# Optimization experiments

Hardware: AMD Instinct MI355X
Metric: run time of the kernel (lower is better)

The kernel has to match this reference:

```python
import jax, jax.numpy as jnp
import numpy as np

DIM = 768
NUM_HEADS = 12
HEAD_DIM = DIM // NUM_HEADS
SCALE = HEAD_DIM ** -0.5


def setup_inputs() -> dict:
    key = jax.random.key(0)
    k1, k2, k3, k4 = jax.random.split(key, 4)
    B, N, C = 4, 2048, DIM
    x = jax.random.normal(k1, (B, N, C), dtype=jnp.float32)
    # nn.Linear(dim, 3*dim, bias=False): weight shape (3C, C), y = x @ W^T
    w_qkv = jax.random.normal(k2, (3 * C, C), dtype=jnp.float32) * (C ** -0.5)
    # nn.Linear(dim, dim) with default bias=True
    w_proj = jax.random.normal(k3, (C, C), dtype=jnp.float32) * (C ** -0.5)
    b_proj = jax.random.normal(k4, (C,), dtype=jnp.float32) * 0.02
    return {"x": x, "w_qkv": w_qkv, "w_proj": w_proj, "b_proj": b_proj}


def reference(x, w_qkv, w_proj, b_proj):
    B, N, C = x.shape
    H, D = NUM_HEADS, HEAD_DIM
    qkv = jnp.einsum('bnc,oc->bno', x, w_qkv)  # (B, N, 3C)
    qkv = qkv.reshape(B, N, 3, H, D).transpose(2, 0, 3, 1, 4)  # (3, B, H, N, D)
    q, k, v = qkv[0], qkv[1], qkv[2]
    attn = jnp.einsum('bhnd,bhmd->bhnm', q, k) * jnp.float32(SCALE)  # (B,H,N,N)
    attn = jax.nn.softmax(attn, axis=-1)
    out = jnp.einsum('bhnm,bhmd->bhnd', attn, v)  # (B,H,N,D)
    out = out.transpose(0, 2, 1, 3).reshape(B, N, C)
    out = jnp.einsum('bnc,oc->bno', out, w_proj) + b_proj
    return out
```

## Files before the change

### kernel.cpp

```cpp
#include <hip/hip_runtime.h>
#include <math.h>

#define B_ 4
#define N_ 2048
#define C_ 768
#define H_ 12
#define D_ 64
#define SCALE_ 0.125f

typedef unsigned short u16;
typedef unsigned int u32;
typedef short s16x8 __attribute__((ext_vector_type(8)));
typedef float f32x4 __attribute__((ext_vector_type(4)));

__device__ __forceinline__ u16 f2bf(float f) {
    union { float f; unsigned int u; } v; v.f = f;
    unsigned int r = (v.u + 0x7fffu + ((v.u >> 16) & 1u)) >> 16;
    return (u16)r;
}

__global__ __launch_bounds__(256) void cvt_bf16(const float4* __restrict__ src,
                                                ushort4* __restrict__ dst, int n4)
{
    int i = blockIdx.x * blockDim.x + threadIdx.x;
    const int stride = gridDim.x * blockDim.x;
    for (; i < n4; i += stride) {
        float4 v = src[i];
        ushort4 o;
        o.x = f2bf(v.x); o.y = f2bf(v.y); o.z = f2bf(v.z); o.w = f2bf(v.w);
        dst[i] = o;
    }
}

template<bool OUT_BF16, bool BIAS, bool QSCALE>
__global__ __launch_bounds__(256) void gemm_mfma(const u16* __restrict__ A,
                                                 const u16* __restrict__ Bm,
                                                 const float* __restrict__ bias,
                                                 void* __restrict__ Cout,
                                                 int M, int N, int K)
{
    __shared__ u16 As[128][40];
    __shared__ u16 Bs[128][40];
    const int tid  = threadIdx.x;
    const int wv   = tid >> 6;
    const int lane = tid & 63;
    const int lr   = lane & 15;
    const int lq   = lane >> 4;
    const int wm   = (wv >> 1) * 64, wn = (wv & 1) * 64;
    const int row0 = blockIdx.y * 128, col0 = blockIdx.x * 128;

    f32x4 acc[4][4];
    #pragma unroll
    for (int i = 0; i < 4; i++)
        #pragma unroll
        for (int j = 0; j < 4; j++) { f32x4 z = {0.f,0.f,0.f,0.f}; acc[i][j] = z; }

    const int srow = tid >> 1, scol = (tid & 1) * 16;
    const u16* Ag = A + (size_t)(row0 + srow) * K + scol;
    const u16* Bg = Bm + (size_t)(col0 + srow) * K + scol;

    for (int k0 = 0; k0 < K; k0 += 32) {
        *(s16x8*)&As[srow][scol]     = *(const s16x8*)(Ag + k0);
        *(s16x8*)&As[srow][scol + 8] = *(const s16x8*)(Ag + k0 + 8);
        *(s16x8*)&Bs[srow][scol]     = *(const s16x8*)(Bg + k0);
        *(s16x8*)&Bs[srow][scol + 8] = *(const s16x8*)(Bg + k0 + 8);
        __syncthreads();
        s16x8 af[4], bfr[4];
        #pragma unroll
        for (int i = 0; i < 4; i++) af[i]  = *(const s16x8*)&As[wm + 16*i + lr][lq*8];
        #pragma unroll
        for (int j = 0; j < 4; j++) bfr[j] = *(const s16x8*)&Bs[wn + 16*j + lr][lq*8];
        #pragma unroll
        for (int i = 0; i < 4; i++)
            #pragma unroll
            for (int j = 0; j < 4; j++)
                acc[i][j] = __builtin_amdgcn_mfma_f32_16x16x32_bf16(af[i], bfr[j], acc[i][j], 0, 0, 0);
        __syncthreads();
    }

    #pragma unroll
    for (int i = 0; i < 4; i++) {
        #pragma unroll
        for (int j = 0; j < 4; j++) {
            const int col = col0 + wn + 16*j + lr;
            float bv = BIAS ? bias[col] : 0.f;
            #pragma unroll
            for (int r = 0; r < 4; r++) {
                const int row = row0 + wm + 16*i + lq*4 + r;
                float v = acc[i][j][r] + bv;
                if (QSCALE && col < C_) v *= SCALE_;
                if (OUT_BF16) ((u16*)Cout)[(size_t)row * N + col] = f2bf(v);
                else          ((float*)Cout)[(size_t)row * N + col] = v;
            }
        }
    }
}

__global__ __launch_bounds__(256, 4) void attn_mfma(const u16* __restrict__ qkv,
                                                    u16* __restrict__ attout)
{
    __shared__ u16 Ks[64][72];
    __shared__ u16 Vt[64][72];
    __shared__ u16 Ps[128][72];

    const int tid  = threadIdx.x;
    const int wv   = tid >> 6;
    const int lane = tid & 63;
    const int lr   = lane & 15;
    const int lq   = lane >> 4;
    const int n0   = blockIdx.x * 128;
    const int bh   = blockIdx.y, b = bh / H_, h = bh % H_;
    const size_t rs = 3 * C_;

    const u16* Qg = qkv + ((size_t)b * N_ + n0) * rs + h * D_;
    const u16* Kg = qkv + ((size_t)b * N_) * rs + C_ + h * D_;
    const u16* Vg = Kg + C_;

    s16x8 qf[2][2];
    #pragma unroll
    for (int i = 0; i < 2; i++)
        #pragma unroll
        for (int kk = 0; kk < 2; kk++)
            qf[i][kk] = *(const s16x8*)(Qg + (size_t)(32*wv + 16*i + lr) * rs + kk*32 + lq*8);

    f32x4 oacc[2][4];
    float li[2][4];
    #pragma unroll
    for (int i = 0; i < 2; i++) {
        #pragma unroll
        for (int j = 0; j < 4; j++) { f32x4 z = {0.f,0.f,0.f,0.f}; oacc[i][j] = z; }
        #pragma unroll
        for (int r = 0; r < 4; r++) li[i][r] = 0.f;
    }

    const int skey = tid >> 2, sd0 = (tid & 3) * 16;
    const int vc = tid & 7, vp = tid >> 3;
    const int vkey0 = 2 * vp, vd0 = vc * 8;
    const int vcol0 = (vkey0 + 8 * vc) & 63;

    for (int t = 0; t < N_ / 64; t++) {
        __syncthreads();
        const u16* ksrc = Kg + (size_t)(t * 64 + skey) * rs + sd0;
        *(s16x8*)&Ks[skey][sd0]     = *(const s16x8*)(ksrc);
        *(s16x8*)&Ks[skey][sd0 + 8] = *(const s16x8*)(ksrc + 8);
        const u16* vsrc = Vg + (size_t)(t * 64 + vkey0) * rs + vd0;
        s16x8 v0 = *(const s16x8*)(vsrc);
        s16x8 v1 = *(const s16x8*)(vsrc + rs);
        #pragma unroll
        for (int u = 0; u < 8; u++) {
            u32 pk = (u32)(u16)v0[u] | ((u32)(u16)v1[u] << 16);
            *(u32*)&Vt[vd0 + u][vcol0] = pk;
        }
        __syncthreads();

        f32x4 sacc[2][4];
        #pragma unroll
        for (int i = 0; i < 2; i++)
            #pragma unroll
            for (int j = 0; j < 4; j++) { f32x4 z = {0.f,0.f,0.f,0.f}; sacc[i][j] = z; }
        #pragma unroll
        for (int kk = 0; kk < 2; kk++) {
            s16x8 bk[4];
            #pragma unroll
            for (int j = 0; j < 4; j++)
                bk[j] = *(const s16x8*)&Ks[16*j + lr][kk*32 + lq*8];
            #pragma unroll
            for (int j = 0; j < 4; j++) {
                sacc[0][j] = __builtin_amdgcn_mfma_f32_16x16x32_bf16(qf[0][kk], bk[j], sacc[0][j], 0, 0, 0);
                sacc[1][j] = __builtin_amdgcn_mfma_f32_16x16x32_bf16(qf[1][kk], bk[j], sacc[1][j], 0, 0, 0);
            }
        }

        #pragma unroll
        for (int i = 0; i < 2; i++)
            #pragma unroll
            for (int j = 0; j < 4; j++)
                #pragma unroll
                for (int r = 0; r < 4; r++) {
                    const float p = __expf(sacc[i][j][r]);
                    li[i][r] += p;
                    Ps[32*wv + 16*i + lq*4 + r][16*j + lr] = f2bf(p);
                }

        #pragma unroll
        for (int kk = 0; kk < 2; kk++) {
            s16x8 ap0 = *(const s16x8*)&Ps[32*wv      + lr][kk*32 + lq*8];
            s16x8 ap1 = *(const s16x8*)&Ps[32*wv + 16 + lr][kk*32 + lq*8];
            #pragma unroll
            for (int j2 = 0; j2 < 4; j2++) {
                const int pb = ((kk*4 + lq) + 2*j2 + (lr >> 3)) & 7;
                s16x8 bv = *(const s16x8*)&Vt[16*j2 + lr][pb * 8];
                oacc[0][j2] = __builtin_amdgcn_mfma_f32_16x16x32_bf16(ap0, bv, oacc[0][j2], 0, 0, 0);
                oacc[1][j2] = __builtin_amdgcn_mfma_f32_16x16x32_bf16(ap1, bv, oacc[1][j2], 0, 0, 0);
            }
        }
    }

    #pragma unroll
    for (int i = 0; i < 2; i++) {
        #pragma unroll
        for (int r = 0; r < 4; r++) {
            float s = li[i][r];
            #pragma unroll
            for (int mask = 1; mask < 16; mask <<= 1)
                s += __shfl_xor(s, mask);
            const float inv = 1.f / s;
            const int row = n0 + 32*wv + 16*i + lq*4 + r;
            #pragma unroll
            for (int j2 = 0; j2 < 4; j2++)
                attout[((size_t)(b * N_ + row)) * C_ + h * D_ + 16*j2 + lr] =
                    f2bf(oacc[i][j2][r] * inv);
        }
    }
}

extern "C" void kernel_launch(void* const* d_in, const int* in_sizes, int n_in,
                              void* d_out, int out_size, void* d_ws, size_t ws_size,
                              hipStream_t stream) {
    const float* x      = (const float*)d_in[0];
    const float* w_qkv  = (const float*)d_in[1];
    const float* w_proj = (const float*)d_in[2];
    const float* b_proj = (const float*)d_in[3];
    float* out = (float*)d_out;

    const int NX = B_ * N_ * C_;
    const int NWQ = 3 * C_ * C_;
    const int NWP = C_ * C_;
    const int NQKV = B_ * N_ * 3 * C_;

    u16* xb   = (u16*)d_ws;
    u16* wqb  = xb + NX;
    u16* wpb  = wqb + NWQ;
    u16* qkvb = wpb + NWP;
    u16* attb = qkvb + NQKV;

    dim3 blk(256);

    cvt_bf16<<<512, blk, 0, stream>>>((const float4*)x, (ushort4*)xb, NX / 4);
    cvt_bf16<<<256, blk, 0, stream>>>((const float4*)w_qkv, (ushort4*)wqb, NWQ / 4);
    cvt_bf16<<<128, blk, 0, stream>>>((const float4*)w_proj, (ushort4*)wpb, NWP / 4);

    const int M = B_ * N_;
    gemm_mfma<true, false, true><<<dim3((3*C_)/128, M/128), blk, 0, stream>>>(
        xb, wqb, nullptr, qkvb, M, 3*C_, C_);

    attn_mfma<<<dim3(N_/128, B_ * H_), blk, 0, stream>>>(qkvb, attb);

    gemm_mfma<false, true, false><<<dim3(C_/128, M/128), blk, 0, stream>>>(
        attb, wpb, b_proj, out, M, C_, C_);
}
```

Before: 252.1 us.

## Use direct global-to-LDS loads in GEMM, prefetch K/V, exp2 softmax with transposed scores

GEMM tiles are now staged with global_load_lds into an XOR-swizzled unpadded LDS layout, and the projection GEMM uses 64-row tiles so more blocks are launched. The attention kernel prefetches the next K/V tile into registers during compute and computes S transposed so each lane holds consecutive keys. That lets P be packed into bf16 pairs with perm and stored as 8-byte writes, and the row-sum reduction becomes two shuffles. The log2(e) factor is folded into the Q scale so exp2 can be used, and the occupancy hint is lowered from 4 to 3 to make room for the prefetch registers. Softmax still skips max-subtraction, so it relies on bounded scores.

```diff
diff --git a/kernel.cpp b/kernel.cpp
--- a/kernel.cpp
+++ b/kernel.cpp
@@ -6,17 +6,31 @@
 #define C_ 768
 #define H_ 12
 #define D_ 64
-#define SCALE_ 0.125f
+#define QKSCALE_ 0.18033688011112042f
 
 typedef unsigned short u16;
 typedef unsigned int u32;
 typedef short s16x8 __attribute__((ext_vector_type(8)));
 typedef float f32x4 __attribute__((ext_vector_type(4)));
+typedef u32 u32x2 __attribute__((ext_vector_type(2)));
 
 __device__ __forceinline__ u16 f2bf(float f) {
-    union { float f; unsigned int u; } v; v.f = f;
-    unsigned int r = (v.u + 0x7fffu + ((v.u >> 16) & 1u)) >> 16;
+    union { float f; u32 u; } v; v.f = f;
+    u32 r = (v.u + 0x7fffu + ((v.u >> 16) & 1u)) >> 16;
     return (u16)r;
+}
+
+__device__ __forceinline__ u32 pkbf(float a, float b) {
+    union { float f; u32 u; } ua, ub; ua.f = a; ub.f = b;
+    u32 ra = ua.u + 0x7fffu + ((ua.u >> 16) & 1u);
+    u32 rb = ub.u + 0x7fffu + ((ub.u >> 16) & 1u);
+    return __builtin_amdgcn_perm(rb, ra, 0x07060302u);
+}
+
+__device__ __forceinline__ void gl_lds16(const u16* g, u16* l) {
+    __builtin_amdgcn_global_load_lds(
+        (__attribute__((address_space(1))) void*)g,
+        (__attribute__((address_space(3))) void*)l, 16, 0, 0);
 }
 
 __global__ __launch_bounds__(256) void cvt_bf16(const float4* __restrict__ src,
@@ -32,46 +46,61 @@
     }
 }
 
-template<bool OUT_BF16, bool BIAS, bool QSCALE>
+template<int BM, bool OUT_BF16, bool BIAS, bool QSCALE>
 __global__ __launch_bounds__(256) void gemm_mfma(const u16* __restrict__ A,
                                                  const u16* __restrict__ Bm,
                                                  const float* __restrict__ bias,
                                                  void* __restrict__ Cout,
                                                  int M, int N, int K)
 {
-    __shared__ u16 As[128][40];
-    __shared__ u16 Bs[128][40];
+    constexpr int MF = BM / 32;
+    __shared__ __align__(16) u16 As[BM * 32];
+    __shared__ __align__(16) u16 Bs[128 * 32];
     const int tid  = threadIdx.x;
     const int wv   = tid >> 6;
     const int lane = tid & 63;
     const int lr   = lane & 15;
     const int lq   = lane >> 4;
-    const int wm   = (wv >> 1) * 64, wn = (wv & 1) * 64;
-    const int row0 = blockIdx.y * 128, col0 = blockIdx.x * 128;
-
-    f32x4 acc[4][4];
-    #pragma unroll
-    for (int i = 0; i < 4; i++)
+    const int wm   = (wv >> 1) * (BM / 2);
+    const int wn   = (wv & 1) * 64;
+    const int row0 = blockIdx.y * BM, col0 = blockIdx.x * 128;
+
+    f32x4 acc[MF][4];
+    #pragma unroll
+    for (int i = 0; i < MF; i++)
         #pragma unroll
         for (int j = 0; j < 4; j++) { f32x4 z = {0.f,0.f,0.f,0.f}; acc[i][j] = z; }
 
-    const int srow = tid >> 1, scol = (tid & 1) * 16;
-    const u16* Ag = A + (size_t)(row0 + srow) * K + scol;
-    const u16* Bg = Bm + (size_t)(col0 + srow) * K + scol;
+    const int srow   = lane >> 2;
+    const int schunk = (((lane & 3) ^ ((lane >> 3) & 3)) * 8);
+
+    const int arow_base = (BM == 128) ? 32 * wv : 16 * wv;
+    const u16* gA0 = A + (size_t)(row0 + arow_base + srow) * K + schunk;
+    const u16* gA1 = gA0 + (size_t)16 * K;
+    const u16* gB0 = Bm + (size_t)(col0 + 32 * wv + srow) * K + schunk;
+    const u16* gB1 = gB0 + (size_t)16 * K;
+    u16* lA0 = As + arow_base * 32;
+    u16* lA1 = lA0 + 16 * 32;
+    u16* lB0 = Bs + (32 * wv) * 32;
+    u16* lB1 = lB0 + 16 * 32;
+
+    const int ppos = (lq ^ ((lr >> 1) & 3)) * 8;
 
     for (int k0 = 0; k0 < K; k0 += 32) {
-        *(s16x8*)&As[srow][scol]     = *(const s16x8*)(Ag + k0);
-        *(s16x8*)&As[srow][scol + 8] = *(const s16x8*)(Ag + k0 + 8);
-        *(s16x8*)&Bs[srow][scol]     = *(const s16x8*)(Bg + k0);
-        *(s16x8*)&Bs[srow][scol + 8] = *(const s16x8*)(Bg + k0 + 8);
-        __syncthreads();
-        s16x8 af[4], bfr[4];
-        #pragma unroll
-        for (int i = 0; i < 4; i++) af[i]  = *(const s16x8*)&As[wm + 16*i + lr][lq*8];
-        #pragma unroll
-        for (int j = 0; j < 4; j++) bfr[j] = *(const s16x8*)&Bs[wn + 16*j + lr][lq*8];
-        #pragma unroll
-        for (int i = 0; i < 4; i++)
+        gl_lds16(gA0 + k0, lA0);
+        if (BM == 128) gl_lds16(gA1 + k0, lA1);
+        gl_lds16(gB0 + k0, lB0);
+        gl_lds16(gB1 + k0, lB1);
+        __syncthreads();
+        s16x8 af[MF], bfr[4];
+        #pragma unroll
+        for (int i = 0; i < MF; i++)
+            af[i] = *(const s16x8*)&As[(wm + 16*i + lr) * 32 + ppos];
+        #pragma unroll
+        for (int j = 0; j < 4; j++)
+            bfr[j] = *(const s16x8*)&Bs[(wn + 16*j + lr) * 32 + ppos];
+        #pragma unroll
+        for (int i = 0; i < MF; i++)
             #pragma unroll
             for (int j = 0; j < 4; j++)
                 acc[i][j] = __builtin_amdgcn_mfma_f32_16x16x32_bf16(af[i], bfr[j], acc[i][j], 0, 0, 0);
@@ -79,7 +108,7 @@
     }
 
     #pragma unroll
-    for (int i = 0; i < 4; i++) {
+    for (int i = 0; i < MF; i++) {
         #pragma unroll
         for (int j = 0; j < 4; j++) {
             const int col = col0 + wn + 16*j + lr;
@@ -88,7 +117,7 @@
             for (int r = 0; r < 4; r++) {
                 const int row = row0 + wm + 16*i + lq*4 + r;
                 float v = acc[i][j][r] + bv;
-                if (QSCALE && col < C_) v *= SCALE_;
+                if (QSCALE && col < C_) v *= QKSCALE_;
                 if (OUT_BF16) ((u16*)Cout)[(size_t)row * N + col] = f2bf(v);
                 else          ((float*)Cout)[(size_t)row * N + col] = v;
             }
@@ -96,12 +125,12 @@
     }
 }
 
-__global__ __launch_bounds__(256, 4) void attn_mfma(const u16* __restrict__ qkv,
+__global__ __launch_bounds__(256, 3) void attn_mfma(const u16* __restrict__ qkv,
                                                     u16* __restrict__ attout)
 {
-    __shared__ u16 Ks[64][72];
-    __shared__ u16 Vt[64][72];
-    __shared__ u16 Ps[128][72];
+    __shared__ __align__(16) u16 Ks[64][72];
+    __shared__ __align__(16) u16 Vt[64][72];
+    __shared__ __align__(16) u16 Ps[128][72];
 
     const int tid  = threadIdx.x;
     const int wv   = tid >> 6;
@@ -118,69 +147,80 @@
 
     s16x8 qf[2][2];
     #pragma unroll
+    for (int iq = 0; iq < 2; iq++)
+        #pragma unroll
+        for (int kk = 0; kk < 2; kk++)
+            qf[iq][kk] = *(const s16x8*)(Qg + (size_t)(32*wv + 16*iq + lr) * rs + kk*32 + lq*8);
+
+    f32x4 oacc[2][4];
+    float li[2] = {0.f, 0.f};
+    #pragma unroll
     for (int i = 0; i < 2; i++)
         #pragma unroll
-        for (int kk = 0; kk < 2; kk++)
-            qf[i][kk] = *(const s16x8*)(Qg + (size_t)(32*wv + 16*i + lr) * rs + kk*32 + lq*8);
-
-    f32x4 oacc[2][4];
-    float li[2][4];
-    #pragma unroll
-    for (int i = 0; i < 2; i++) {
-        #pragma unroll
         for (int j = 0; j < 4; j++) { f32x4 z = {0.f,0.f,0.f,0.f}; oacc[i][j] = z; }
-        #pragma unroll
-        for (int r = 0; r < 4; r++) li[i][r] = 0.f;
-    }
 
     const int skey = tid >> 2, sd0 = (tid & 3) * 16;
     const int vc = tid & 7, vp = tid >> 3;
     const int vkey0 = 2 * vp, vd0 = vc * 8;
     const int vcol0 = (vkey0 + 8 * vc) & 63;
 
+    s16x8 kr0, kr1, vr0, vr1;
+    {
+        const u16* kp = Kg + (size_t)skey * rs + sd0;
+        kr0 = *(const s16x8*)kp; kr1 = *(const s16x8*)(kp + 8);
+        const u16* vp2 = Vg + (size_t)vkey0 * rs + vd0;
+        vr0 = *(const s16x8*)vp2; vr1 = *(const s16x8*)(vp2 + rs);
+    }
+
     for (int t = 0; t < N_ / 64; t++) {
         __syncthreads();
-        const u16* ksrc = Kg + (size_t)(t * 64 + skey) * rs + sd0;
-        *(s16x8*)&Ks[skey][sd0]     = *(const s16x8*)(ksrc);
-        *(s16x8*)&Ks[skey][sd0 + 8] = *(const s16x8*)(ksrc + 8);
-        const u16* vsrc = Vg + (size_t)(t * 64 + vkey0) * rs + vd0;
-        s16x8 v0 = *(const s16x8*)(vsrc);
-        s16x8 v1 = *(const s16x8*)(vsrc + rs);
+        *(s16x8*)&Ks[skey][sd0]     = kr0;
+        *(s16x8*)&Ks[skey][sd0 + 8] = kr1;
         #pragma unroll
         for (int u = 0; u < 8; u++) {
-            u32 pk = (u32)(u16)v0[u] | ((u32)(u16)v1[u] << 16);
+            u32 pk = (u32)(u16)vr0[u] | ((u32)(u16)vr1[u] << 16);
             *(u32*)&Vt[vd0 + u][vcol0] = pk;
         }
         __syncthreads();
-
-        f32x4 sacc[2][4];
-        #pragma unroll
-        for (int i = 0; i < 2; i++)
-            #pragma unroll
-            for (int j = 0; j < 4; j++) { f32x4 z = {0.f,0.f,0.f,0.f}; sacc[i][j] = z; }
+        if (t + 1 < N_ / 64) {
+            const u16* kp = Kg + (size_t)((t+1)*64 + skey) * rs + sd0;
+            kr0 = *(const s16x8*)kp; kr1 = *(const s16x8*)(kp + 8);
+            const u16* vp2 = Vg + (size_t)((t+1)*64 + vkey0) * rs + vd0;
+            vr0 = *(const s16x8*)vp2; vr1 = *(const s16x8*)(vp2 + rs);
+        }
+
+        f32x4 st[4][2];
+        #pragma unroll
+        for (int jk = 0; jk < 4; jk++)
+            #pragma unroll
+            for (int iq = 0; iq < 2; iq++) { f32x4 z = {0.f,0.f,0.f,0.f}; st[jk][iq] = z; }
         #pragma unroll
         for (int kk = 0; kk < 2; kk++) {
-            s16x8 bk[4];
-            #pragma unroll
-            for (int j = 0; j < 4; j++)
-                bk[j] = *(const s16x8*)&Ks[16*j + lr][kk*32 + lq*8];
-            #pragma unroll
-            for (int j = 0; j < 4; j++) {
-                sacc[0][j] = __builtin_amdgcn_mfma_f32_16x16x32_bf16(qf[0][kk], bk[j], sacc[0][j], 0, 0, 0);
-                sacc[1][j] = __builtin_amdgcn_mfma_f32_16x16x32_bf16(qf[1][kk], bk[j], sacc[1][j], 0, 0, 0);
-            }
-        }
-
-        #pragma unroll
-        for (int i = 0; i < 2; i++)
-            #pragma unroll
-            for (int j = 0; j < 4; j++)
-                #pragma unroll
-                for (int r = 0; r < 4; r++) {
-                    const float p = __expf(sacc[i][j][r]);
-                    li[i][r] += p;
-                    Ps[32*wv + 16*i + lq*4 + r][16*j + lr] = f2bf(p);
-                }
+            s16x8 kf[4];
+            #pragma unroll
+            for (int jk = 0; jk < 4; jk++)
+                kf[jk] = *(const s16x8*)&Ks[16*jk + lr][kk*32 + lq*8];
+            #pragma unroll
+            for (int jk = 0; jk < 4; jk++) {
+                st[jk][0] = __builtin_amdgcn_mfma_f32_16x16x32_bf16(kf[jk], qf[0][kk], st[jk][0], 0, 0, 0);
+                st[jk][1] = __builtin_amdgcn_mfma_f32_16x16x32_bf16(kf[jk], qf[1][kk], st[jk][1], 0, 0, 0);
+            }
+        }
+
+        #pragma unroll
+        for (int jk = 0; jk < 4; jk++)
+            #pragma unroll
+            for (int iq = 0; iq < 2; iq++) {
+                const float p0 = __builtin_amdgcn_exp2f(st[jk][iq][0]);
+                const float p1 = __builtin_amdgcn_exp2f(st[jk][iq][1]);
+                const float p2 = __builtin_amdgcn_exp2f(st[jk][iq][2]);
+                const float p3 = __builtin_amdgcn_exp2f(st[jk][iq][3]);
+                li[iq] += (p0 + p1) + (p2 + p3);
+                u32x2 w;
+                w.x = pkbf(p0, p1);
+                w.y = pkbf(p2, p3);
+                *(u32x2*)&Ps[32*wv + 16*iq + lr][16*jk + 4*lq] = w;
+            }
 
         #pragma unroll
         for (int kk = 0; kk < 2; kk++) {
@@ -197,19 +237,20 @@
     }
 
     #pragma unroll
-    for (int i = 0; i < 2; i++) {
+    for (int iq = 0; iq < 2; iq++) {
+        li[iq] += __shfl_xor(li[iq], 16);
+        li[iq] += __shfl_xor(li[iq], 32);
+    }
+    #pragma unroll
+    for (int iq = 0; iq < 2; iq++) {
         #pragma unroll
         for (int r = 0; r < 4; r++) {
-            float s = li[i][r];
-            #pragma unroll
-            for (int mask = 1; mask < 16; mask <<= 1)
-                s += __shfl_xor(s, mask);
-            const float inv = 1.f / s;
-            const int row = n0 + 32*wv + 16*i + lq*4 + r;
+            const float inv = 1.f / __shfl(li[iq], 4*lq + r);
+            const int row = n0 + 32*wv + 16*iq + 4*lq + r;
             #pragma unroll
             for (int j2 = 0; j2 < 4; j2++)
                 attout[((size_t)(b * N_ + row)) * C_ + h * D_ + 16*j2 + lr] =
-                    f2bf(oacc[i][j2][r] * inv);
+                    f2bf(oacc[iq][j2][r] * inv);
         }
     }
 }
@@ -223,9 +264,9 @@
     const float* b_proj = (const float*)d_in[3];
     float* out = (float*)d_out;
 
-    const int NX = B_ * N_ * C_;
-    const int NWQ = 3 * C_ * C_;
-    const int NWP = C_ * C_;
+    const int NX   = B_ * N_ * C_;
+    const int NWQ  = 3 * C_ * C_;
+    const int NWP  = C_ * C_;
     const int NQKV = B_ * N_ * 3 * C_;
 
     u16* xb   = (u16*)d_ws;
@@ -241,11 +282,11 @@
     cvt_bf16<<<128, blk, 0, stream>>>((const float4*)w_proj, (ushort4*)wpb, NWP / 4);
 
     const int M = B_ * N_;
-    gemm_mfma<true, false, true><<<dim3((3*C_)/128, M/128), blk, 0, stream>>>(
+    gemm_mfma<128, true, false, true><<<dim3((3*C_)/128, M/128), blk, 0, stream>>>(
         xb, wqb, nullptr, qkvb, M, 3*C_, C_);
 
     attn_mfma<<<dim3(N_/128, B_ * H_), blk, 0, stream>>>(qkvb, attb);
 
-    gemm_mfma<false, true, false><<<dim3(C_/128, M/128), blk, 0, stream>>>(
+    gemm_mfma<64, false, true, false><<<dim3(C_/128, M/64), blk, 0, stream>>>(
         attb, wpb, b_proj, out, M, C_, C_);
 }
```

Result: faster. 232.9 us (-7.6%).
